# Optimization experiments

Measured on AMD Instinct MI355X. Metric: run time of the kernel, lower is better.

## Reference

```python
import jax, jax.numpy as jnp
import numpy as np

TOP_K = 2
EPS = 1e-6

def setup_inputs() -> dict:
    key = jax.random.key(0)
    ks = jax.random.split(key, 6)
    Bt, S, D, E, R = 4, 4096, 1024, 8, 4
    s = lambda d: 1.0 / np.sqrt(d)
    return {
        "x": jax.random.normal(ks[0], (Bt, S, D), jnp.float32),
        "W_base": jax.random.normal(ks[1], (D, D), jnp.float32) * s(D),
        "b_base": jax.random.normal(ks[2], (D,), jnp.float32) * 0.02,
        "W_router": jax.random.normal(ks[3], (E, D), jnp.float32) * s(D),
        "A": jax.random.normal(ks[4], (E, D, R), jnp.float32) * s(D),
        "B": jax.random.normal(ks[5], (E, R, D), jnp.float32) * s(R),
    }

def reference(x, W_base, b_base, W_router, A, B):
    # frozen base linear: [b,s,d] @ [out,d]^T + bias
    base_out = jnp.einsum('bsd,od->bso', x, W_base) + b_base
    # router softmax gate over experts
    logits = jnp.einsum('bsd,ed->bse', x, W_router)
    gate = jax.nn.softmax(logits, axis=-1)
    # top-k scatter-mask (values kept are the gate values themselves)
    topv, topi = jax.lax.top_k(gate, TOP_K)                    # [b,s,k]
    mask = jnp.sum(jax.nn.one_hot(topi, gate.shape[-1], dtype=gate.dtype), axis=-2)
    gate = gate * mask
    gate = gate / (jnp.sum(gate, axis=-1, keepdims=True) + EPS)
    # batched rank-4 LoRA experts, gating applied in low-rank space
    h = jnp.einsum('bsd,edr->bser', x, A)                      # [b,s,E,r]
    hg = h * gate[..., None]                                   # weight before up-proj
    lora_out = jnp.einsum('bser,ero->bso', hg, B)
    return base_out + lora_out
```

## Files before the change

### kernel.cpp

```cpp
#include <hip/hip_runtime.h>
#include <cstdint>

typedef __attribute__((ext_vector_type(8))) short short8;
typedef __attribute__((ext_vector_type(4))) float f32x4;

__device__ inline unsigned short f2bf(float f){
  union { float f; uint32_t u; } v; v.f = f;
  uint32_t r = v.u + 0x7FFFu + ((v.u >> 16) & 1u);
  return (unsigned short)(r >> 16);
}

#define GLL(gp, lp) __builtin_amdgcn_global_load_lds(              \
    (const __attribute__((address_space(1))) void*)(gp),           \
    (__attribute__((address_space(3))) void*)(lp), 16, 0, 0)

#define DSR(dst, addr) asm volatile("ds_read_b128 %0, %1" : "=v"(dst) : "v"(addr))

__global__ __launch_bounds__(256) void kconv(const float* __restrict__ W,
                                             const float* __restrict__ A,
                                             const float* __restrict__ Bm,
                                             unsigned short* __restrict__ Wb,
                                             unsigned short* __restrict__ BTt,
                                             unsigned short* __restrict__ W2b){
  int i = blockIdx.x * 256 + threadIdx.x;
  Wb[i] = f2bf(W[i]);
  if (i < 32768){
    int o = i >> 5, c = i & 31;
    BTt[i] = f2bf(Bm[(size_t)c*1024 + o]);
    int n = i >> 10, d = i & 1023;
    W2b[i] = f2bf(A[(((size_t)(n>>2))*1024 + d)*4 + (n&3)]);
  }
}

__global__ __launch_bounds__(256) void kxl2(const float* __restrict__ x,
                                            const float* __restrict__ Wr,
                                            unsigned short* __restrict__ xb,
                                            float* __restrict__ gate){
  __shared__ float wr[8192];
  const int tid  = threadIdx.x;
  const int lane = tid & 63;
  const int wid  = tid >> 6;
  {
    const float4* s  = (const float4*)Wr;
    float4*       d4 = (float4*)wr;
    #pragma unroll
    for (int j=0;j<8;j++) d4[j*256+tid] = s[j*256+tid];
  }
  __syncthreads();
  const int tk  = lane >> 3, ln8 = lane & 7;
  const size_t tok = (size_t)blockIdx.x*32 + wid*8 + tk;
  const float4* xr = (const float4*)(x + tok*1024);
  ushort4*      xd = (ushort4*)(xb + tok*1024);
  const float4* wv = (const float4*)wr;
  float p[8] = {0.f,0.f,0.f,0.f,0.f,0.f,0.f,0.f};
  #pragma unroll 4
  for (int it=0; it<32; it++){
    float4 v = xr[it*8 + ln8];
    ushort4 o; o.x=f2bf(v.x); o.y=f2bf(v.y); o.z=f2bf(v.z); o.w=f2bf(v.w);
    xd[it*8 + ln8] = o;
    #pragma unroll
    for (int e=0;e<8;e++){
      float4 wq = wv[e*256 + it*8 + ln8];
      p[e] += v.x*wq.x + v.y*wq.y + v.z*wq.z + v.w*wq.w;
    }
  }
  #pragma unroll
  for (int off=1; off<8; off<<=1){
    #pragma unroll
    for (int e=0;e<8;e++) p[e] += __shfl_xor(p[e], off, 64);
  }
  if (ln8 == 0){
    float mx = p[0];
    #pragma unroll
    for (int e=1;e<8;e++) mx = fmaxf(mx, p[e]);
    float ex[8], s2 = 0.f;
    #pragma unroll
    for (int e=0;e<8;e++){ ex[e] = __expf(p[e]-mx); s2 += ex[e]; }
    int i1 = 0; float v1 = ex[0];
    #pragma unroll
    for (int e=1;e<8;e++) if (ex[e] > v1){ v1 = ex[e]; i1 = e; }
    int i2 = -1; float v2 = -1.f;
    #pragma unroll
    for (int e=0;e<8;e++) if (e != i1 && ex[e] > v2){ v2 = ex[e]; i2 = e; }
    float g1 = v1/s2, g2 = v2/s2;
    float rs = 1.f/(g1 + g2 + 1e-6f);
    float* go = gate + tok*8;
    #pragma unroll
    for (int e=0;e<8;e++) go[e] = (e==i1 ? g1 : (e==i2 ? g2 : 0.f)) * rs;
  }
}

__global__ __launch_bounds__(256) void kh(const unsigned short* __restrict__ xbp,
                                          const unsigned short* __restrict__ W2b,
                                          const float* __restrict__ gate,
                                          unsigned short* __restrict__ HG){
  const int tid  = threadIdx.x;
  const int lane = tid & 63;
  const int wid  = tid >> 6;
  const int lrow = lane & 15;
  const int lk   = (lane >> 4) * 8;
  const int tok0 = blockIdx.x*64 + wid*16;
  f32x4 acc0 = {0.f,0.f,0.f,0.f}, acc1 = {0.f,0.f,0.f,0.f};
  const unsigned short* b0 = W2b + (size_t)lrow*1024 + lk;
  const unsigned short* b1 = W2b + (size_t)(16+lrow)*1024 + lk;
  const unsigned short* ar = xbp + (size_t)(tok0+lrow)*1024 + lk;
  #pragma unroll 4
  for (int ks=0; ks<32; ks++){
    short8 av  = *(const short8*)(ar + ks*32);
    short8 bv0 = *(const short8*)(b0 + ks*32);
    short8 bv1 = *(const short8*)(b1 + ks*32);
    acc0 = __builtin_amdgcn_mfma_f32_16x16x32_bf16(av, bv0, acc0, 0, 0, 0);
    acc1 = __builtin_amdgcn_mfma_f32_16x16x32_bf16(av, bv1, acc1, 0, 0, 0);
  }
  #pragma unroll
  for (int j=0;j<4;j++){
    int tok = tok0 + (lane>>4)*4 + j;
    float g0 = gate[(size_t)tok*8 + (lrow>>2)];
    float g1 = gate[(size_t)tok*8 + 4 + (lrow>>2)];
    HG[(size_t)tok*32 + lrow]      = f2bf(acc0[j]*g0);
    HG[(size_t)tok*32 + 16 + lrow] = f2bf(acc1[j]*g1);
  }
}

__global__ __launch_bounds__(512, 2) void kgemm5(const unsigned short* __restrict__ xb,
                                                 const unsigned short* __restrict__ Wb,
                                                 const unsigned short* __restrict__ BTt,
                                                 const unsigned short* __restrict__ HG,
                                                 const float* __restrict__ bias,
                                                 float* __restrict__ out){
  __shared__ __attribute__((aligned(128))) char lds[131072];
  char* ldsc = lds;
  const uint32_t L = (uint32_t)(uintptr_t)lds;
  const int tid  = threadIdx.x;
  const int lane = tid & 63;
  const int w    = tid >> 6;
  const int xcd  = blockIdx.x & 7, jj = blockIdx.x >> 3;
  const int nblk = xcd >> 1;
  const int mblk = (xcd & 1)*32 + jj;
  const int m0 = mblk << 8, n0 = nblk << 8;
  const int wm = w >> 2, wn = w & 3;
  const int lrow = lane & 15;
  const int q    = lane >> 4;

  const int swzk = (lrow & 7) << 4;
  uint32_t offA[8], offB[4];
  #pragma unroll
  for (int fm=0; fm<8; fm++){ int r = wm*128 + fm*16 + lrow; offA[fm] = r*128 + ((q<<4) ^ swzk); }
  #pragma unroll
  for (int fn=0; fn<4; fn++){ int r = wn*64  + fn*16 + lrow; offB[fn] = r*128 + ((q<<4) ^ swzk); }

  const int rowL = lane >> 3;
  const int colb = ((lane & 7) ^ rowL) << 4;
  const int rbA = (w>>2)*128 + (w&3)*16;
  const int rbB = (w>>1)*64 + (w&1)*16;
  const char* Ag = (const char*)xb + ((size_t)(m0 + rbA + rowL) << 11) + colb;
  const char* Bg = (const char*)Wb + ((size_t)(n0 + rbB + rowL) << 11) + colb;

#define STG_A(tt, h, ss) do{                                                    \
    GLL(Ag + (size_t)(h)*131072 + (tt)*128,                                     \
        ldsc + (ss)*32768 + (rbA + (h)*64)*128 + lane*16);                      \
    GLL(Ag + (size_t)(h)*131072 + 16384 + (tt)*128,                             \
        ldsc + (ss)*32768 + (rbA + (h)*64 + 8)*128 + lane*16); }while(0)
#define STG_B(tt, h, ss) do{                                                    \
    GLL(Bg + (size_t)(h)*65536 + (tt)*128,                                      \
        ldsc + 65536 + (ss)*32768 + (rbB + (h)*32)*128 + lane*16);              \
    GLL(Bg + (size_t)(h)*65536 + 16384 + (tt)*128,                              \
        ldsc + 65536 + (ss)*32768 + (rbB + (h)*32 + 8)*128 + lane*16); }while(0)

  f32x4 acc[8][4];
  #pragma unroll
  for (int a2=0;a2<8;a2++)
    #pragma unroll
    for (int b2=0;b2<4;b2++) acc[a2][b2] = (f32x4){0.f,0.f,0.f,0.f};

  STG_A(0,0,0); STG_A(0,1,0); STG_B(0,0,0); STG_B(0,1,0);
  asm volatile("s_waitcnt vmcnt(0)" ::: "memory");
  __builtin_amdgcn_s_barrier();

  short8 a[8], b0[4], b1[4];
  #pragma unroll 1
  for (int t = 0; t < 16; ++t){
    const int s = t & 1, sn = s ^ 1;
    const uint32_t bA = L + s*32768;
    const uint32_t bB = L + 65536 + s*32768;
    #pragma unroll
    for (int fm=0; fm<4; fm++){ DSR(a[fm*2], bA+offA[fm]); DSR(a[fm*2+1], bA+(offA[fm]^64u)); }
    #pragma unroll
    for (int fn=0; fn<2; fn++){ DSR(b0[fn*2], bB+offB[fn]); DSR(b0[fn*2+1], bB+(offB[fn]^64u)); }
    if (t < 15){ STG_A(t+1, 0, sn); asm volatile("s_waitcnt vmcnt(2)" ::: "memory"); }
    else       {                    asm volatile("s_waitcnt vmcnt(0)" ::: "memory"); }
    __builtin_amdgcn_s_barrier();
    asm volatile("s_waitcnt lgkmcnt(0)" ::: "memory");
    __builtin_amdgcn_sched_barrier(0);
    __builtin_amdgcn_s_setprio(1);
    #pragma unroll
    for (int kk=0;kk<2;kk++)
      #pragma unroll
      for (int fm=0;fm<4;fm++)
        #pragma unroll
        for (int fn=0;fn<2;fn++)
          acc[fm][fn] = __builtin_amdgcn_mfma_f32_16x16x32_bf16(a[fm*2+kk], b0[fn*2+kk], acc[fm][fn], 0, 0, 0);
    __builtin_amdgcn_s_setprio(0);
    __builtin_amdgcn_s_barrier();
    #pragma unroll
    for (int fn=0; fn<2; fn++){ DSR(b1[fn*2], bB+offB[2+fn]); DSR(b1[fn*2+1], bB+(offB[2+fn]^64u)); }
    if (t < 15) STG_A(t+1, 1, sn);
    __builtin_amdgcn_s_barrier();
    asm volatile("s_waitcnt lgkmcnt(0)" ::: "memory");
    __builtin_amdgcn_sched_barrier(0);
    __builtin_amdgcn_s_setprio(1);
    #pragma unroll
    for (int kk=0;kk<2;kk++)
      #pragma unroll
      for (int fm=0;fm<4;fm++)
        #pragma unroll
        for (int fn=0;fn<2;fn++)
          acc[fm][2+fn] = __builtin_amdgcn_mfma_f32_16x16x32_bf16(a[fm*2+kk], b1[fn*2+kk], acc[fm][2+fn], 0, 0, 0);
    __builtin_amdgcn_s_setprio(0);
    __builtin_amdgcn_s_barrier();
    #pragma unroll
    for (int fm=0; fm<4; fm++){ DSR(a[fm*2], bA+offA[4+fm]); DSR(a[fm*2+1], bA+(offA[4+fm]^64u)); }
    if (t < 15) STG_B(t+1, 0, sn);
    __builtin_amdgcn_s_barrier();
    asm volatile("s_waitcnt lgkmcnt(0)" ::: "memory");
    __builtin_amdgcn_sched_barrier(0);
    __builtin_amdgcn_s_setprio(1);
    #pragma unroll
    for (int kk=0;kk<2;kk++)
      #pragma unroll
      for (int fm=0;fm<4;fm++)
        #pragma unroll
        for (int fn=0;fn<2;fn++)
          acc[4+fm][2+fn] = __builtin_amdgcn_mfma_f32_16x16x32_bf16(a[fm*2+kk], b1[fn*2+kk], acc[4+fm][2+fn], 0, 0, 0);
    __builtin_amdgcn_s_setprio(0);
    __builtin_amdgcn_s_barrier();
    if (t < 15){ STG_B(t+1, 1, sn); asm volatile("s_waitcnt vmcnt(2)" ::: "memory"); }
    __builtin_amdgcn_s_barrier();
    __builtin_amdgcn_s_setprio(1);
    #pragma unroll
    for (int kk=0;kk<2;kk++)
      #pragma unroll
      for (int fm=0;fm<4;fm++)
        #pragma unroll
        for (int fn=0;fn<2;fn++)
          acc[4+fm][fn] = __builtin_amdgcn_mfma_f32_16x16x32_bf16(a[fm*2+kk], b0[fn*2+kk], acc[4+fm][fn], 0, 0, 0);
    __builtin_amdgcn_s_setprio(0);
    __builtin_amdgcn_s_barrier();
  }

  {
    const int colb2 = (((lane & 3) ^ ((lane >> 3) & 3)) << 4);
    const char* Hg = (const char*)HG  + (size_t)(m0 + w*32 + (lane>>2))*64 + colb2;
    const char* Tg = (const char*)BTt + (size_t)(n0 + w*32 + (lane>>2))*64 + colb2;
    const int dst2 = w*2048 + lane*16;
    GLL(Hg,        ldsc + dst2);
    GLL(Hg + 1024, ldsc + dst2 + 1024);
    GLL(Tg,        ldsc + 65536 + dst2);
    GLL(Tg + 1024, ldsc + 65536 + dst2 + 1024);
    asm volatile("s_waitcnt vmcnt(0)" ::: "memory");
    __builtin_amdgcn_s_barrier();
    const int swz2 = ((lrow >> 1) & 3) << 4;
    short8 hb[4];
    #pragma unroll
    for (int fn=0; fn<4; fn++){
      int r = wn*64 + fn*16 + lrow;
      hb[fn] = *(const short8*)(ldsc + 65536 + r*64 + ((q<<4) ^ swz2));
    }
    #pragma unroll
    for (int fm=0; fm<8; fm++){
      int r = wm*128 + fm*16 + lrow;
      short8 ha = *(const short8*)(ldsc + r*64 + ((q<<4) ^ swz2));
      #pragma unroll
      for (int fn=0; fn<4; fn++)
        acc[fm][fn] = __builtin_amdgcn_mfma_f32_16x16x32_bf16(ha, hb[fn], acc[fm][fn], 0, 0, 0);
    }
  }

  #pragma unroll
  for (int fn=0;fn<4;fn++){
    int col = n0 + wn*64 + fn*16 + lrow;
    float bv = bias[col];
    #pragma unroll
    for (int fm=0;fm<8;fm++){
      int rb = m0 + wm*128 + fm*16 + q*4;
      #pragma unroll
      for (int j=0;j<4;j++)
        out[(size_t)(rb+j)*1024 + col] = acc[fm][fn][j] + bv;
    }
  }
#undef STG_A
#undef STG_B
}

extern "C" void kernel_launch(void* const* d_in, const int* in_sizes, int n_in,
                              void* d_out, int out_size, void* d_ws, size_t ws_size,
                              hipStream_t stream){
  const float* x  = (const float*)d_in[0];
  const float* W  = (const float*)d_in[1];
  const float* bb = (const float*)d_in[2];
  const float* Wr = (const float*)d_in[3];
  const float* A  = (const float*)d_in[4];
  const float* Bm = (const float*)d_in[5];
  float* out = (float*)d_out;
  char* ws = (char*)d_ws;

  unsigned short* Wb   = (unsigned short*)(ws + 0);
  unsigned short* BTt  = (unsigned short*)(ws + 2097152);
  unsigned short* W2b  = (unsigned short*)(ws + 2162688);
  float*          gate = (float*)         (ws + 2228224);
  unsigned short* HG   = (unsigned short*)(ws + 2752512);
  unsigned short* xb   = (unsigned short*)(ws + 3801088);

  kconv<<<4096, 256, 0, stream>>>(W, A, Bm, Wb, BTt, W2b);
  kxl2<<<512, 256, 0, stream>>>(x, Wr, xb, gate);
  kh<<<256, 256, 0, stream>>>(xb, W2b, gate, HG);
  kgemm5<<<256, 512, 0, stream>>>(xb, Wb, BTt, HG, bb, out);
}
```

Baseline: 91.21 us.

## Fuse LoRA down-projection into main GEMM, reusing staged x tiles

Removes the separate kh kernel and computes the rank-32 LoRA down-projection inside the main GEMM loop. It reuses the x fragments already loaded into LDS and reads the A weights directly from global memory. The gated low-rank activations are formed in LDS after the loop, and the up-projection runs from LDS with B read from global. LDS reads now use immediate offsets, and the XCD-aware block mapping is replaced by a plain m/n mapping. This saves a kernel launch and a second full read of x, but it adds MFMA work per tile, since the down-projection is recomputed for each of the 4 n-blocks, and the simpler block mapping may lose L2 locality.

```diff
diff --git a/kernel.cpp b/kernel.cpp
--- a/kernel.cpp
+++ b/kernel.cpp
@@ -14,7 +14,8 @@
     (const __attribute__((address_space(1))) void*)(gp),           \
     (__attribute__((address_space(3))) void*)(lp), 16, 0, 0)
 
-#define DSR(dst, addr) asm volatile("ds_read_b128 %0, %1" : "=v"(dst) : "v"(addr))
+#define DSRO(dst, addr, off) \
+  asm volatile("ds_read_b128 %0, %1 offset:" off : "=v"(dst) : "v"(addr))
 
 __global__ __launch_bounds__(256) void kconv(const float* __restrict__ W,
                                              const float* __restrict__ A,
@@ -90,42 +91,11 @@
   }
 }
 
-__global__ __launch_bounds__(256) void kh(const unsigned short* __restrict__ xbp,
-                                          const unsigned short* __restrict__ W2b,
-                                          const float* __restrict__ gate,
-                                          unsigned short* __restrict__ HG){
-  const int tid  = threadIdx.x;
-  const int lane = tid & 63;
-  const int wid  = tid >> 6;
-  const int lrow = lane & 15;
-  const int lk   = (lane >> 4) * 8;
-  const int tok0 = blockIdx.x*64 + wid*16;
-  f32x4 acc0 = {0.f,0.f,0.f,0.f}, acc1 = {0.f,0.f,0.f,0.f};
-  const unsigned short* b0 = W2b + (size_t)lrow*1024 + lk;
-  const unsigned short* b1 = W2b + (size_t)(16+lrow)*1024 + lk;
-  const unsigned short* ar = xbp + (size_t)(tok0+lrow)*1024 + lk;
-  #pragma unroll 4
-  for (int ks=0; ks<32; ks++){
-    short8 av  = *(const short8*)(ar + ks*32);
-    short8 bv0 = *(const short8*)(b0 + ks*32);
-    short8 bv1 = *(const short8*)(b1 + ks*32);
-    acc0 = __builtin_amdgcn_mfma_f32_16x16x32_bf16(av, bv0, acc0, 0, 0, 0);
-    acc1 = __builtin_amdgcn_mfma_f32_16x16x32_bf16(av, bv1, acc1, 0, 0, 0);
-  }
-  #pragma unroll
-  for (int j=0;j<4;j++){
-    int tok = tok0 + (lane>>4)*4 + j;
-    float g0 = gate[(size_t)tok*8 + (lrow>>2)];
-    float g1 = gate[(size_t)tok*8 + 4 + (lrow>>2)];
-    HG[(size_t)tok*32 + lrow]      = f2bf(acc0[j]*g0);
-    HG[(size_t)tok*32 + 16 + lrow] = f2bf(acc1[j]*g1);
-  }
-}
-
-__global__ __launch_bounds__(512, 2) void kgemm5(const unsigned short* __restrict__ xb,
+__global__ __launch_bounds__(512, 2) void kgemm6(const unsigned short* __restrict__ xb,
                                                  const unsigned short* __restrict__ Wb,
                                                  const unsigned short* __restrict__ BTt,
-                                                 const unsigned short* __restrict__ HG,
+                                                 const unsigned short* __restrict__ W2b,
+                                                 const float* __restrict__ gate,
                                                  const float* __restrict__ bias,
                                                  float* __restrict__ out){
   __shared__ __attribute__((aligned(128))) char lds[131072];
@@ -134,20 +104,18 @@
   const int tid  = threadIdx.x;
   const int lane = tid & 63;
   const int w    = tid >> 6;
-  const int xcd  = blockIdx.x & 7, jj = blockIdx.x >> 3;
-  const int nblk = xcd >> 1;
-  const int mblk = (xcd & 1)*32 + jj;
+  const int mblk = blockIdx.x & 63;
+  const int nblk = blockIdx.x >> 6;
   const int m0 = mblk << 8, n0 = nblk << 8;
   const int wm = w >> 2, wn = w & 3;
   const int lrow = lane & 15;
   const int q    = lane >> 4;
 
   const int swzk = (lrow & 7) << 4;
-  uint32_t offA[8], offB[4];
-  #pragma unroll
-  for (int fm=0; fm<8; fm++){ int r = wm*128 + fm*16 + lrow; offA[fm] = r*128 + ((q<<4) ^ swzk); }
-  #pragma unroll
-  for (int fn=0; fn<4; fn++){ int r = wn*64  + fn*16 + lrow; offB[fn] = r*128 + ((q<<4) ^ swzk); }
+  const uint32_t vA0 = L + (uint32_t)(wm*128 + lrow)*128 + (uint32_t)((q<<4) ^ swzk);
+  const uint32_t vA1 = L + (uint32_t)(wm*128 + lrow)*128 + (uint32_t)(((q^4)<<4) ^ swzk);
+  const uint32_t vB0 = L + 65536u + (uint32_t)(wn*64 + lrow)*128 + (uint32_t)((q<<4) ^ swzk);
+  const uint32_t vB1 = L + 65536u + (uint32_t)(wn*64 + lrow)*128 + (uint32_t)(((q^4)<<4) ^ swzk);
 
   const int rowL = lane >> 3;
   const int colb = ((lane & 7) ^ rowL) << 4;
@@ -172,6 +140,11 @@
   for (int a2=0;a2<8;a2++)
     #pragma unroll
     for (int b2=0;b2<4;b2++) acc[a2][b2] = (f32x4){0.f,0.f,0.f,0.f};
+  f32x4 acc_h[4];
+  #pragma unroll
+  for (int f=0; f<4; f++) acc_h[f] = (f32x4){0.f,0.f,0.f,0.f};
+
+  const unsigned short* c2p = W2b + (size_t)((wn&1)*16 + lrow)*1024 + q*8;
 
   STG_A(0,0,0); STG_A(0,1,0); STG_B(0,0,0); STG_B(0,1,0);
   asm volatile("s_waitcnt vmcnt(0)" ::: "memory");
@@ -181,12 +154,17 @@
   #pragma unroll 1
   for (int t = 0; t < 16; ++t){
     const int s = t & 1, sn = s ^ 1;
-    const uint32_t bA = L + s*32768;
-    const uint32_t bB = L + 65536 + s*32768;
-    #pragma unroll
-    for (int fm=0; fm<4; fm++){ DSR(a[fm*2], bA+offA[fm]); DSR(a[fm*2+1], bA+(offA[fm]^64u)); }
-    #pragma unroll
-    for (int fn=0; fn<2; fn++){ DSR(b0[fn*2], bB+offB[fn]); DSR(b0[fn*2+1], bB+(offB[fn]^64u)); }
+    const uint32_t va0 = vA0 + s*32768, va1 = vA1 + s*32768;
+    const uint32_t vb0 = vB0 + s*32768, vb1 = vB1 + s*32768;
+    short8 c2[2];
+    c2[0] = *(const short8*)(c2p + t*64);
+    c2[1] = *(const short8*)(c2p + t*64 + 32);
+    DSRO(a[0], va0, "0");    DSRO(a[1], va1, "0");
+    DSRO(a[2], va0, "2048"); DSRO(a[3], va1, "2048");
+    DSRO(a[4], va0, "4096"); DSRO(a[5], va1, "4096");
+    DSRO(a[6], va0, "6144"); DSRO(a[7], va1, "6144");
+    DSRO(b0[0], vb0, "0");    DSRO(b0[1], vb1, "0");
+    DSRO(b0[2], vb0, "2048"); DSRO(b0[3], vb1, "2048");
     if (t < 15){ STG_A(t+1, 0, sn); asm volatile("s_waitcnt vmcnt(2)" ::: "memory"); }
     else       {                    asm volatile("s_waitcnt vmcnt(0)" ::: "memory"); }
     __builtin_amdgcn_s_barrier();
@@ -202,8 +180,8 @@
           acc[fm][fn] = __builtin_amdgcn_mfma_f32_16x16x32_bf16(a[fm*2+kk], b0[fn*2+kk], acc[fm][fn], 0, 0, 0);
     __builtin_amdgcn_s_setprio(0);
     __builtin_amdgcn_s_barrier();
-    #pragma unroll
-    for (int fn=0; fn<2; fn++){ DSR(b1[fn*2], bB+offB[2+fn]); DSR(b1[fn*2+1], bB+(offB[2+fn]^64u)); }
+    DSRO(b1[0], vb0, "4096"); DSRO(b1[1], vb1, "4096");
+    DSRO(b1[2], vb0, "6144"); DSRO(b1[3], vb1, "6144");
     if (t < 15) STG_A(t+1, 1, sn);
     __builtin_amdgcn_s_barrier();
     asm volatile("s_waitcnt lgkmcnt(0)" ::: "memory");
@@ -216,10 +194,19 @@
         #pragma unroll
         for (int fn=0;fn<2;fn++)
           acc[fm][2+fn] = __builtin_amdgcn_mfma_f32_16x16x32_bf16(a[fm*2+kk], b1[fn*2+kk], acc[fm][2+fn], 0, 0, 0);
+    if (wn < 2){
+      #pragma unroll
+      for (int kk=0;kk<2;kk++)
+        #pragma unroll
+        for (int f=0;f<4;f++)
+          acc_h[f] = __builtin_amdgcn_mfma_f32_16x16x32_bf16(a[f*2+kk], c2[kk], acc_h[f], 0, 0, 0);
+    }
     __builtin_amdgcn_s_setprio(0);
     __builtin_amdgcn_s_barrier();
-    #pragma unroll
-    for (int fm=0; fm<4; fm++){ DSR(a[fm*2], bA+offA[4+fm]); DSR(a[fm*2+1], bA+(offA[4+fm]^64u)); }
+    DSRO(a[0], va0, "8192");  DSRO(a[1], va1, "8192");
+    DSRO(a[2], va0, "10240"); DSRO(a[3], va1, "10240");
+    DSRO(a[4], va0, "12288"); DSRO(a[5], va1, "12288");
+    DSRO(a[6], va0, "14336"); DSRO(a[7], va1, "14336");
     if (t < 15) STG_B(t+1, 0, sn);
     __builtin_amdgcn_s_barrier();
     asm volatile("s_waitcnt lgkmcnt(0)" ::: "memory");
@@ -244,32 +231,45 @@
         #pragma unroll
         for (int fn=0;fn<2;fn++)
           acc[4+fm][fn] = __builtin_amdgcn_mfma_f32_16x16x32_bf16(a[fm*2+kk], b0[fn*2+kk], acc[4+fm][fn], 0, 0, 0);
+    if (wn >= 2){
+      #pragma unroll
+      for (int kk=0;kk<2;kk++)
+        #pragma unroll
+        for (int f=0;f<4;f++)
+          acc_h[f] = __builtin_amdgcn_mfma_f32_16x16x32_bf16(a[f*2+kk], c2[kk], acc_h[f], 0, 0, 0);
+    }
     __builtin_amdgcn_s_setprio(0);
     __builtin_amdgcn_s_barrier();
   }
 
+  __syncthreads();
   {
-    const int colb2 = (((lane & 3) ^ ((lane >> 3) & 3)) << 4);
-    const char* Hg = (const char*)HG  + (size_t)(m0 + w*32 + (lane>>2))*64 + colb2;
-    const char* Tg = (const char*)BTt + (size_t)(n0 + w*32 + (lane>>2))*64 + colb2;
-    const int dst2 = w*2048 + lane*16;
-    GLL(Hg,        ldsc + dst2);
-    GLL(Hg + 1024, ldsc + dst2 + 1024);
-    GLL(Tg,        ldsc + 65536 + dst2);
-    GLL(Tg + 1024, ldsc + 65536 + dst2 + 1024);
-    asm volatile("s_waitcnt vmcnt(0)" ::: "memory");
-    __builtin_amdgcn_s_barrier();
-    const int swz2 = ((lrow >> 1) & 3) << 4;
+    float4* gl4 = (float4*)(ldsc + 24576);
+    gl4[tid] = ((const float4*)(gate + (size_t)m0*8))[tid];
+  }
+  __syncthreads();
+  unsigned short* HGl = (unsigned short*)ldsc;
+  const float*    gl  = (const float*)(ldsc + 24576);
+  {
+    const int rbase = wm*128 + (wn>>1)*64;
+    const int n = (wn&1)*16 + lrow;
+    #pragma unroll
+    for (int f=0; f<4; f++)
+      #pragma unroll
+      for (int j=0;j<4;j++){
+        int row = rbase + f*16 + q*4 + j;
+        HGl[row*40 + n] = f2bf(acc_h[f][j] * gl[row*8 + (n>>2)]);
+      }
+  }
+  __syncthreads();
+  {
     short8 hb[4];
     #pragma unroll
-    for (int fn=0; fn<4; fn++){
-      int r = wn*64 + fn*16 + lrow;
-      hb[fn] = *(const short8*)(ldsc + 65536 + r*64 + ((q<<4) ^ swz2));
-    }
+    for (int fn=0; fn<4; fn++)
+      hb[fn] = *(const short8*)(BTt + (size_t)(n0 + wn*64 + fn*16 + lrow)*32 + q*8);
     #pragma unroll
     for (int fm=0; fm<8; fm++){
-      int r = wm*128 + fm*16 + lrow;
-      short8 ha = *(const short8*)(ldsc + r*64 + ((q<<4) ^ swz2));
+      short8 ha = *(const short8*)((const char*)HGl + (size_t)(wm*128 + fm*16 + lrow)*80 + q*16);
       #pragma unroll
       for (int fn=0; fn<4; fn++)
         acc[fm][fn] = __builtin_amdgcn_mfma_f32_16x16x32_bf16(ha, hb[fn], acc[fm][fn], 0, 0, 0);
@@ -308,11 +308,9 @@
   unsigned short* BTt  = (unsigned short*)(ws + 2097152);
   unsigned short* W2b  = (unsigned short*)(ws + 2162688);
   float*          gate = (float*)         (ws + 2228224);
-  unsigned short* HG   = (unsigned short*)(ws + 2752512);
-  unsigned short* xb   = (unsigned short*)(ws + 3801088);
+  unsigned short* xb   = (unsigned short*)(ws + 2752512);
 
   kconv<<<4096, 256, 0, stream>>>(W, A, Bm, Wb, BTt, W2b);
   kxl2<<<512, 256, 0, stream>>>(x, Wr, xb, gate);
-  kh<<<256, 256, 0, stream>>>(xb, W2b, gate, HG);
-  kgemm5<<<256, 512, 0, stream>>>(xb, Wb, BTt, HG, bb, out);
-}
+  kgemm6<<<256, 512, 0, stream>>>(xb, Wb, BTt, W2b, gate, bb, out);
+}
```

After: 86.85 us. 4.8% less time.
